# Optimization experiments

Hardware: AMD Instinct MI355X
Metric: run time of the kernel (lower is better)

## Reference

```python
import jax, jax.numpy as jnp
import numpy as np

B, N, F, DM, DMO, OM, L = 32, 64, 64, 128, 64, 128, 4
PRE_H, PRE_O, POST_H = 128, 64, 64
E = N * N
EPS = 1e-5


def swish(x):
    return x * jax.nn.sigmoid(x)


def bn_edges(x, g, b):
    # BatchNorm1d(num_features=E) applied to [B, E, D]: per-edge-channel stats over (batch, D)
    m = x.mean(axis=(0, 2), keepdims=True)
    v = x.var(axis=(0, 2), keepdims=True)
    return (x - m) / jnp.sqrt(v + EPS) * g[None, :, None] + b[None, :, None]


def setup_inputs():
    key = jax.random.key(0)
    ks = iter(jax.random.split(key, 64))

    def rn(shape, s=0.05):
        return jax.random.normal(next(ks), shape, dtype=jnp.float32) * s

    # fully-connected graph incl. self-loops (required by BatchNorm1d(n_nodes^2))
    src, dst = np.meshgrid(np.arange(N), np.arange(N), indexing='ij')
    edge_index = jnp.asarray(np.stack([src.reshape(-1), dst.reshape(-1)]), dtype=jnp.int32)
    return {
        'node_feature': rn((B, N, F), 1.0),
        'vectors': rn((B, N, OM), 1.0),
        'edge_index': edge_index,
        'msg_W1': rn((L, 2 * F, DM)), 'msg_b1': rn((L, DM)),
        'bn1_g': jnp.ones((L, E), jnp.float32), 'bn1_b': jnp.zeros((L, E), jnp.float32),
        'msg_W2': rn((L, DM, DM)), 'msg_b2': rn((L, DM)),
        'bn2_g': jnp.ones((L, E), jnp.float32), 'bn2_b': jnp.zeros((L, E), jnp.float32),
        'msg_W3': rn((L, DM, DM)), 'msg_b3': rn((L, DM)),
        'bn3_g': jnp.ones((L, E), jnp.float32), 'bn3_b': jnp.zeros((L, E), jnp.float32),
        'msg_W4': rn((L, DM, DMO)), 'msg_b4': rn((L, DMO)),
        'upd_W1': rn((L, OM + F + DMO, DM)), 'upd_b1': rn((L, DM)),
        'upd_W2': rn((L, DM, DM)), 'upd_b2': rn((L, DM)),
        'upd_W3': rn((L, DM, DM)), 'upd_b3': rn((L, DM)),
        'upd_W4': rn((L, DM, F)), 'upd_b4': rn((L, F)),
        'pre_W1': rn((F, PRE_H)), 'pre_b1': rn((PRE_H,)),
        'pre_W2': rn((PRE_H, PRE_H)), 'pre_b2': rn((PRE_H,)),
        'pre_W3': rn((PRE_H, PRE_H)), 'pre_b3': rn((PRE_H,)),
        'pre_W4': rn((PRE_H, PRE_O)), 'pre_b4': rn((PRE_O,)),
        'post_W1': rn((PRE_O, POST_H)), 'post_b1': rn((POST_H,)),
        'post_W2': rn((POST_H, 1)), 'post_b2': rn((1,)),
    }


def reference(node_feature, vectors, edge_index,
              msg_W1, msg_b1, bn1_g, bn1_b, msg_W2, msg_b2, bn2_g, bn2_b,
              msg_W3, msg_b3, bn3_g, bn3_b, msg_W4, msg_b4,
              upd_W1, upd_b1, upd_W2, upd_b2, upd_W3, upd_b3, upd_W4, upd_b4,
              pre_W1, pre_b1, pre_W2, pre_b2, pre_W3, pre_b3, pre_W4, pre_b4,
              post_W1, post_b1, post_W2, post_b2):
    src, dst = edge_index[0], edge_index[1]
    x = node_feature  # [B, N, F]
    v = vectors       # [B, N, OM]
    cnt = jax.ops.segment_sum(jnp.ones((E,), jnp.float32), dst, num_segments=N)
    inv_cnt = 1.0 / jnp.maximum(cnt, 1.0)
    for l in range(L):
        x_i = x[:, dst]  # [B, E, F] gather targets
        x_j = x[:, src]  # [B, E, F] gather sources
        h = swish(jnp.concatenate([x_i, x_j], -1) @ msg_W1[l] + msg_b1[l])
        h = bn_edges(h, bn1_g[l], bn1_b[l])
        h = bn_edges(swish(h @ msg_W2[l] + msg_b2[l]), bn2_g[l], bn2_b[l])
        h = bn_edges(swish(h @ msg_W3[l] + msg_b3[l]), bn3_g[l], bn3_b[l])
        m = swish(h @ msg_W4[l] + msg_b4[l])  # [B, E, DMO]
        agg = jax.ops.segment_sum(jnp.transpose(m, (1, 0, 2)), dst, num_segments=N)
        agg = jnp.transpose(agg, (1, 0, 2)) * inv_cnt[None, :, None]  # mean aggr, [B, N, DMO]
        u = jnp.concatenate([v, x, agg], -1)  # [B, N, OM+F+DMO]
        h = swish(u @ upd_W1[l] + upd_b1[l])
        h = swish(h @ upd_W2[l] + upd_b2[l])
        h = swish(h @ upd_W3[l] + upd_b3[l])
        x = x + swish(h @ upd_W4[l] + upd_b4[l])  # residual update
    h = swish(x @ pre_W1 + pre_b1)
    h = swish(h @ pre_W2 + pre_b2)
    h = swish(h @ pre_W3 + pre_b3)
    h = h @ pre_W4 + pre_b4
    c = swish(h @ post_W1 + post_b1) @ post_W2 + post_b2  # [B, N, 1]
    x3 = jnp.einsum('bnd,bn->bd', v, c[..., 0])           # coefficient-weighted vector sum
    return x3, v, c
```

## Files before the change

kernel.cpp:

```cpp
#include <hip/hip_runtime.h>
#include <hip/hip_bf16.h>

typedef unsigned short u16t;
typedef __attribute__((ext_vector_type(8))) short bf16x8;
typedef __attribute__((ext_vector_type(4))) float f32x4;

#define Bn 32
#define Nn 64
#define Fd 64
#define DMd 128
#define DMOd 64
#define OMd 128
#define En 4096

#define NTEN 36
#define TOTALC 1073217
#define HP 136
#define UP 264
#define XP 72
#define WSEG 131072

__device__ const int kOffs[NTEN + 1] = {
    0,        131072,   393216,   458752,   459264,   475648,   492032,   557568,
    558080,   574464,   590848,   656384,   656896,   673280,   689664,   722432,
    722688,   853760,   854272,   919808,   920320,   985856,   986368,   1019136,
    1019392,  1027584,  1027712,  1044096,  1044224,  1060608,  1060736,  1068928,
    1068992,  1073088,  1073152,  1073216,  1073217
};

#define C_NF    0
#define C_VEC   131072
#define C_MW1   393216
#define C_MB1   458752
#define C_G1    459264
#define C_BB1   475648
#define C_MW2   492032
#define C_MB2   557568
#define C_G2    558080
#define C_BB2   574464
#define C_MW3   590848
#define C_MB3   656384
#define C_G3    656896
#define C_BB3   673280
#define C_MW4   689664
#define C_MB4   722432
#define C_UW1   722688
#define C_UB1   853760
#define C_UW2   854272
#define C_UB2   919808
#define C_UW3   920320
#define C_UB3   985856
#define C_UW4   986368
#define C_UB4   1019136
#define C_PW1   1019392
#define C_PB1   1027584
#define C_PW2   1027712
#define C_PB2   1044096
#define C_PW3   1044224
#define C_PB3   1060608
#define C_PW4   1060736
#define C_PB4   1068928
#define C_QW1   1068992
#define C_QB1   1073088
#define C_QW2   1073152
#define C_QB2   1073216

#define S_W2T 0
#define S_W3T 16384
#define S_W4T 32768
#define S_U1T 40960
#define S_U2T 73728
#define S_U3T 90112
#define S_U4T 106496
#define S_W1T 114688

struct Ptrs { const void* p[NTEN]; };

__device__ __forceinline__ float us2f(u16t u) {
    return __uint_as_float(((unsigned int)u) << 16);
}
__device__ __forceinline__ u16t f2us(float f) {
    __hip_bfloat16 h = __float2bfloat16(f);
    return *reinterpret_cast<u16t*>(&h);
}
__device__ __forceinline__ u16t f2us_fast(float f) {
    return (u16t)((__float_as_uint(f) + 0x8000u) >> 16);
}
__device__ __forceinline__ unsigned pack2(float f0, float f1) {
    return __builtin_amdgcn_perm(__float_as_uint(f1) + 0x8000u,
                                 __float_as_uint(f0) + 0x8000u, 0x07060302u);
}
__device__ __forceinline__ float swishf(float x) {
    return x * __builtin_amdgcn_rcpf(1.0f + __expf(-x));
}

__global__ void k_flag(const u16t* __restrict__ g1raw, int* __restrict__ flag) {
    if (threadIdx.x == 0) *flag = (g1raw[0] == 0x3F80u) ? 1 : 0;
}

__global__ __launch_bounds__(256) void k_convert(Ptrs t, float* __restrict__ C,
                                                 float* __restrict__ x,
                                                 const int* __restrict__ flagp) {
    int i = blockIdx.x * 256 + threadIdx.x;
    if (i >= TOTALC) return;
    const int flag = *flagp;
    int lo = 0, hi = NTEN;
    while (hi - lo > 1) { int m = (lo + hi) >> 1; if (i >= kOffs[m]) lo = m; else hi = m; }
    const int local = i - kOffs[lo];
    float v;
    if (flag) v = us2f(((const u16t*)t.p[lo])[local]);
    else      v = ((const float*)t.p[lo])[local];
    C[i] = v;
    if (i < Bn * Nn * Fd) x[i] = v;
}

__global__ __launch_bounds__(256) void k_prepw(const float* __restrict__ C,
                                               u16t* __restrict__ W) {
    int i = blockIdx.x * 256 + threadIdx.x;
    if (i >= 4 * WSEG) return;
    const int l = i / WSEG;
    int r = i - l * WSEG;
    int src;
    if (r < S_W3T)      { int q = r;          int n = q >> 7, k = q & 127; src = C_MW2 + l*16384 + k*128 + n; }
    else if (r < S_W4T) { int q = r - S_W3T;  int n = q >> 7, k = q & 127; src = C_MW3 + l*16384 + k*128 + n; }
    else if (r < S_U1T) { int q = r - S_W4T;  int n = q >> 7, k = q & 127; src = C_MW4 + l*8192  + k*64  + n; }
    else if (r < S_U2T) { int q = r - S_U1T;  int n = q >> 8, k = q & 255; src = C_UW1 + l*32768 + k*128 + n; }
    else if (r < S_U3T) { int q = r - S_U2T;  int n = q >> 7, k = q & 127; src = C_UW2 + l*16384 + k*128 + n; }
    else if (r < S_U4T) { int q = r - S_U3T;  int n = q >> 7, k = q & 127; src = C_UW3 + l*16384 + k*128 + n; }
    else if (r < S_W1T) { int q = r - S_U4T;  int n = q >> 7, k = q & 127; src = C_UW4 + l*8192  + k*64  + n; }
    else                { int q = r - S_W1T;  int n = q >> 7, k = q & 127; src = C_MW1 + l*16384 + k*128 + n; }
    W[i] = f2us(C[src]);
}

__global__ __launch_bounds__(128) void k_pq0(const float* __restrict__ x,
                                             const float* __restrict__ W1,
                                             float* __restrict__ P, float* __restrict__ Q,
                                             float* __restrict__ agg) {
    const int gid = blockIdx.x * 128 + threadIdx.x;
    if (gid < Bn * Nn * DMOd) agg[gid] = 0.f;
    __shared__ float xr[Fd];
    const int bn = blockIdx.x;
    const int tid = threadIdx.x;
    if (tid < Fd) xr[tid] = x[bn * Fd + tid];
    __syncthreads();
    float accP = 0.f, accQ = 0.f;
    #pragma unroll
    for (int k = 0; k < Fd; k++) {
        float xv = xr[k];
        accP += xv * W1[k * DMd + tid];
        accQ += xv * W1[(Fd + k) * DMd + tid];
    }
    P[bn * DMd + tid] = accP;
    Q[bn * DMd + tid] = accQ;
}

__device__ __forceinline__ void red8(float* s, float (*red)[8], float (*stats)[2],
                                     int wv, int lane, int tid) {
    #pragma unroll
    for (int off = 32; off > 0; off >>= 1)
        #pragma unroll
        for (int k = 0; k < 8; k++) s[k] += __shfl_down(s[k], off);
    if (lane == 0) {
        #pragma unroll
        for (int k = 0; k < 8; k++) red[wv][k] = s[k];
    }
    __syncthreads();
    if (tid < 4) {
        float S  = red[0][2*tid]   + red[1][2*tid]   + red[2][2*tid]   + red[3][2*tid];
        float S2 = red[0][2*tid+1] + red[1][2*tid+1] + red[2][2*tid+1] + red[3][2*tid+1];
        float mean = S * (1.0f / 4096.0f);
        float var  = S2 * (1.0f / 4096.0f) - mean * mean;
        stats[tid][0] = mean;
        stats[tid][1] = rsqrtf(var + 1e-5f);
    }
    __syncthreads();
}

__global__ __launch_bounds__(256, 4) void k_edge(
    const float* __restrict__ P, const float* __restrict__ Q,
    const float* __restrict__ b1v,
    const float* __restrict__ g1, const float* __restrict__ bb1,
    const u16t* __restrict__ W2t, const float* __restrict__ b2v,
    const float* __restrict__ g2, const float* __restrict__ bb2,
    const u16t* __restrict__ W3t, const float* __restrict__ b3v,
    const float* __restrict__ g3, const float* __restrict__ bb3,
    const u16t* __restrict__ W4t, const float* __restrict__ b4v,
    float* __restrict__ agg) {
    __shared__ u16t hE[4][Bn * HP];
    __shared__ float red[4][8];
    __shared__ float stats[4][2];

    const int dst = blockIdx.x & 63, src0 = (blockIdx.x >> 6) * 4;
    const int tid = threadIdx.x;
    const int wv = tid >> 6, lane = tid & 63, quad = lane >> 4, l15 = lane & 15;
    const int mw = wv & 1, nb2 = wv >> 1;
    const int mrow = mw * 16 + l15;
    const int nBase = nb2 * 64;

    {
        const int b = tid >> 3, d0 = (tid & 7) * 16;
        float4 pv[4], bv[4];
        {
            const float4* pp = (const float4*)&P[(b * Nn + dst) * DMd + d0];
            const float4* bp = (const float4*)&b1v[d0];
            #pragma unroll
            for (int j = 0; j < 4; j++) { pv[j] = pp[j]; bv[j] = bp[j]; }
        }
        float h[4][16];
        #pragma unroll
        for (int e = 0; e < 4; e++) {
            const float4* qq = (const float4*)&Q[(b * Nn + src0 + e) * DMd + d0];
            #pragma unroll
            for (int j = 0; j < 4; j++) {
                float4 qv = qq[j];
                h[e][j*4+0] = swishf(pv[j].x + qv.x + bv[j].x);
                h[e][j*4+1] = swishf(pv[j].y + qv.y + bv[j].y);
                h[e][j*4+2] = swishf(pv[j].z + qv.z + bv[j].z);
                h[e][j*4+3] = swishf(pv[j].w + qv.w + bv[j].w);
            }
        }
        float s[8];
        #pragma unroll
        for (int e = 0; e < 4; e++) {
            float se = 0.f, s2e = 0.f;
            #pragma unroll
            for (int i = 0; i < 16; i++) { se += h[e][i]; s2e += h[e][i] * h[e][i]; }
            s[2*e] = se; s[2*e+1] = s2e;
        }
        red8(s, red, stats, wv, lane, tid);
        #pragma unroll
        for (int e = 0; e < 4; e++) {
            float a  = stats[e][1] * g1[(src0 + e) * Nn + dst];
            float cc = bb1[(src0 + e) * Nn + dst] - stats[e][0] * a;
            uint4 w0, w1;
            w0.x = pack2(h[e][0]  * a + cc, h[e][1]  * a + cc);
            w0.y = pack2(h[e][2]  * a + cc, h[e][3]  * a + cc);
            w0.z = pack2(h[e][4]  * a + cc, h[e][5]  * a + cc);
            w0.w = pack2(h[e][6]  * a + cc, h[e][7]  * a + cc);
            w1.x = pack2(h[e][8]  * a + cc, h[e][9]  * a + cc);
            w1.y = pack2(h[e][10] * a + cc, h[e][11] * a + cc);
            w1.z = pack2(h[e][12] * a + cc, h[e][13] * a + cc);
            w1.w = pack2(h[e][14] * a + cc, h[e][15] * a + cc);
            *(uint4*)&hE[e][b * HP + d0]     = w0;
            *(uint4*)&hE[e][b * HP + d0 + 8] = w1;
        }
    }
    __syncthreads();

    #pragma unroll 1
    for (int st = 0; st < 2; st++) {
        const u16t*  Wt = st ? W3t : W2t;
        const float* bv = st ? b3v : b2v;
        const float* gv = st ? g3  : g2;
        const float* bb = st ? bb3 : bb2;
        f32x4 acc[4][4];
        #pragma unroll
        for (int t = 0; t < 4; t++) {
            float b0 = bv[nBase + t * 16 + l15];
            #pragma unroll
            for (int e = 0; e < 4; e++) acc[e][t] = (f32x4){b0, b0, b0, b0};
        }
        #pragma unroll
        for (int ks = 0; ks < 4; ks++) {
            bf16x8 wb[4];
            #pragma unroll
            for (int t = 0; t < 4; t++)
                wb[t] = *(const bf16x8*)&Wt[(nBase + t * 16 + l15) * 128 + ks * 32 + quad * 8];
            #pragma unroll
            for (int e = 0; e < 4; e++) {
                bf16x8 a8 = *(const bf16x8*)&hE[e][mrow * HP + ks * 32 + quad * 8];
                #pragma unroll
                for (int t = 0; t < 4; t++)
                    acc[e][t] = __builtin_amdgcn_mfma_f32_16x16x32_bf16(a8, wb[t], acc[e][t], 0, 0, 0);
            }
        }
        float s[8];
        #pragma unroll
        for (int e = 0; e < 4; e++) {
            float se = 0.f, s2e = 0.f;
            #pragma unroll
            for (int t = 0; t < 4; t++)
                #pragma unroll
                for (int r = 0; r < 4; r++) {
                    float v = swishf(acc[e][t][r]);
                    acc[e][t][r] = v;
                    se += v; s2e += v * v;
                }
            s[2*e] = se; s[2*e+1] = s2e;
        }
        red8(s, red, stats, wv, lane, tid);
        #pragma unroll
        for (int e = 0; e < 4; e++) {
            float a  = stats[e][1] * gv[(src0 + e) * Nn + dst];
            float cc = bb[(src0 + e) * Nn + dst] - stats[e][0] * a;
            #pragma unroll
            for (int t = 0; t < 4; t++)
                #pragma unroll
                for (int r = 0; r < 4; r++)
                    hE[e][(mw * 16 + quad * 4 + r) * HP + nBase + t * 16 + l15] =
                        f2us_fast(acc[e][t][r] * a + cc);
        }
        __syncthreads();
    }

    {
        const int n40 = nb2 * 32;
        f32x4 a4[4][2];
        #pragma unroll
        for (int t = 0; t < 2; t++) {
            float b0 = b4v[n40 + t * 16 + l15];
            #pragma unroll
            for (int e = 0; e < 4; e++) a4[e][t] = (f32x4){b0, b0, b0, b0};
        }
        #pragma unroll
        for (int ks = 0; ks < 4; ks++) {
            bf16x8 wb[2];
            #pragma unroll
            for (int t = 0; t < 2; t++)
                wb[t] = *(const bf16x8*)&W4t[(n40 + t * 16 + l15) * 128 + ks * 32 + quad * 8];
            #pragma unroll
            for (int e = 0; e < 4; e++) {
                bf16x8 a8 = *(const bf16x8*)&hE[e][mrow * HP + ks * 32 + quad * 8];
                #pragma unroll
                for (int t = 0; t < 2; t++)
                    a4[e][t] = __builtin_amdgcn_mfma_f32_16x16x32_bf16(a8, wb[t], a4[e][t], 0, 0, 0);
            }
        }
        #pragma unroll
        for (int t = 0; t < 2; t++)
            #pragma unroll
            for (int r = 0; r < 4; r++) {
                float m = swishf(a4[0][t][r]) + swishf(a4[1][t][r])
                        + swishf(a4[2][t][r]) + swishf(a4[3][t][r]);
                int b = mw * 16 + quad * 4 + r;
                atomicAdd(&agg[(b * Nn + dst) * DMOd + n40 + t * 16 + l15], m);
            }
    }
}

__global__ __launch_bounds__(256, 4) void k_updq(
    const float* __restrict__ vC, float* __restrict__ x, float* __restrict__ agg,
    const u16t* __restrict__ U1t, const float* __restrict__ b1,
    const u16t* __restrict__ U2t, const float* __restrict__ b2,
    const u16t* __restrict__ U3t, const float* __restrict__ b3,
    const u16t* __restrict__ U4t, const float* __restrict__ b4,
    const u16t* __restrict__ W1Tn, float* __restrict__ Pn, float* __restrict__ Qn,
    int doPQ) {
    __shared__ u16t uL[16 * UP];
    __shared__ u16t hL[16 * HP];
    __shared__ u16t xL[16 * XP];
    const int g0 = blockIdx.x * 16;
    const int tid = threadIdx.x;
    const int wv = tid >> 6, lane = tid & 63, quad = lane >> 4, l15 = lane & 15;
    const int nBase = wv * 32;

    {
        const int i = tid >> 4, c0 = (tid & 15) * 16;
        const int g = g0 + i;
        const float* srcp; float scl = 1.f;
        if (c0 < 128)       srcp = &vC[g * OMd + c0];
        else if (c0 < 192)  srcp = &x[g * Fd + (c0 - 128)];
        else              { srcp = &agg[g * DMOd + (c0 - 192)]; scl = 1.0f / 64.0f; }
        uint4 s0, s1;
        s0.x = pack2(srcp[0]  * scl, srcp[1]  * scl);
        s0.y = pack2(srcp[2]  * scl, srcp[3]  * scl);
        s0.z = pack2(srcp[4]  * scl, srcp[5]  * scl);
        s0.w = pack2(srcp[6]  * scl, srcp[7]  * scl);
        s1.x = pack2(srcp[8]  * scl, srcp[9]  * scl);
        s1.y = pack2(srcp[10] * scl, srcp[11] * scl);
        s1.z = pack2(srcp[12] * scl, srcp[13] * scl);
        s1.w = pack2(srcp[14] * scl, srcp[15] * scl);
        *(uint4*)&uL[i * UP + c0]     = s0;
        *(uint4*)&uL[i * UP + c0 + 8] = s1;
    }
    __syncthreads();

    {
        f32x4 acc[2];
        #pragma unroll
        for (int t = 0; t < 2; t++) {
            float b0 = b1[nBase + t * 16 + l15];
            acc[t] = (f32x4){b0, b0, b0, b0};
        }
        #pragma unroll
        for (int ks = 0; ks < 8; ks++) {
            bf16x8 a8 = *(const bf16x8*)&uL[l15 * UP + ks * 32 + quad * 8];
            #pragma unroll
            for (int t = 0; t < 2; t++) {
                bf16x8 b8 = *(const bf16x8*)&U1t[(nBase + t * 16 + l15) * 256 + ks * 32 + quad * 8];
                acc[t] = __builtin_amdgcn_mfma_f32_16x16x32_bf16(a8, b8, acc[t], 0, 0, 0);
            }
        }
        #pragma unroll
        for (int t = 0; t < 2; t++)
            #pragma unroll
            for (int r = 0; r < 4; r++)
                hL[(quad * 4 + r) * HP + nBase + t * 16 + l15] = f2us_fast(swishf(acc[t][r]));
    }
    __syncthreads();

    #pragma unroll 1
    for (int st = 0; st < 2; st++) {
        const u16t*  Ut = st ? U3t : U2t;
        const float* bb = st ? b3  : b2;
        f32x4 acc[2];
        #pragma unroll
        for (int t = 0; t < 2; t++) {
            float b0 = bb[nBase + t * 16 + l15];
            acc[t] = (f32x4){b0, b0, b0, b0};
        }
        #pragma unroll
        for (int ks = 0; ks < 4; ks++) {
            bf16x8 a8 = *(const bf16x8*)&hL[l15 * HP + ks * 32 + quad * 8];
            #pragma unroll
            for (int t = 0; t < 2; t++) {
                bf16x8 b8 = *(const bf16x8*)&Ut[(nBase + t * 16 + l15) * 128 + ks * 32 + quad * 8];
                acc[t] = __builtin_amdgcn_mfma_f32_16x16x32_bf16(a8, b8, acc[t], 0, 0, 0);
            }
        }
        __syncthreads();
        #pragma unroll
        for (int t = 0; t < 2; t++)
            #pragma unroll
            for (int r = 0; r < 4; r++)
                hL[(quad * 4 + r) * HP + nBase + t * 16 + l15] = f2us_fast(swishf(acc[t][r]));
        __syncthreads();
    }

    {
        const int n4 = wv * 16;
        f32x4 acc;
        {
            float b0 = b4[n4 + l15];
            acc = (f32x4){b0, b0, b0, b0};
        }
        #pragma unroll
        for (int ks = 0; ks < 4; ks++) {
            bf16x8 a8 = *(const bf16x8*)&hL[l15 * HP + ks * 32 + quad * 8];
            bf16x8 b8 = *(const bf16x8*)&U4t[(n4 + l15) * 128 + ks * 32 + quad * 8];
            acc = __builtin_amdgcn_mfma_f32_16x16x32_bf16(a8, b8, acc, 0, 0, 0);
        }
        #pragma unroll
        for (int r = 0; r < 4; r++) {
            int row = quad * 4 + r, col = n4 + l15;
            float xn = x[(g0 + row) * Fd + col] + swishf(acc[r]);
            x[(g0 + row) * Fd + col] = xn;
            xL[row * XP + col] = f2us_fast(xn);
        }
    }

    {
        int idx = tid;
        #pragma unroll
        for (int k = 0; k < 4; k++, idx += 256) agg[g0 * DMOd + idx] = 0.f;
    }
    __syncthreads();

    if (doPQ) {
        f32x4 ap[2], aq[2];
        #pragma unroll
        for (int j = 0; j < 2; j++) { ap[j] = (f32x4){0,0,0,0}; aq[j] = (f32x4){0,0,0,0}; }
        #pragma unroll
        for (int ks = 0; ks < 2; ks++) {
            bf16x8 a8 = *(const bf16x8*)&xL[l15 * XP + ks * 32 + quad * 8];
            #pragma unroll
            for (int j = 0; j < 2; j++) {
                const int n0 = (wv * 2 + j) * 16 + l15;
                bf16x8 bp = *(const bf16x8*)&W1Tn[n0 * 128 + ks * 32 + quad * 8];
                bf16x8 bq = *(const bf16x8*)&W1Tn[n0 * 128 + 64 + ks * 32 + quad * 8];
                ap[j] = __builtin_amdgcn_mfma_f32_16x16x32_bf16(a8, bp, ap[j], 0, 0, 0);
                aq[j] = __builtin_amdgcn_mfma_f32_16x16x32_bf16(a8, bq, aq[j], 0, 0, 0);
            }
        }
        #pragma unroll
        for (int j = 0; j < 2; j++)
            #pragma unroll
            for (int r = 0; r < 4; r++) {
                int g = g0 + quad * 4 + r, col = (wv * 2 + j) * 16 + l15;
                Pn[g * DMd + col] = ap[j][r];
                Qn[g * DMd + col] = aq[j][r];
            }
    }
}

__global__ __launch_bounds__(128) void k_final(
    const float* __restrict__ x, const void* __restrict__ vraw,
    const float* __restrict__ pW1, const float* __restrict__ pb1,
    const float* __restrict__ pW2, const float* __restrict__ pb2,
    const float* __restrict__ pW3, const float* __restrict__ pb3,
    const float* __restrict__ pW4, const float* __restrict__ pb4,
    const float* __restrict__ qW1, const float* __restrict__ qb1,
    const float* __restrict__ qW2, const float* __restrict__ qb2,
    float* __restrict__ c_buf, void* __restrict__ out, const int* __restrict__ flagp) {
    __shared__ float xr[64];
    __shared__ float ha[128];
    __shared__ float hb[128];
    __shared__ float hc[64];
    __shared__ float tt[64];
    const int bn = blockIdx.x;
    const int tid = threadIdx.x;
    const int flag = *flagp;
    if (tid < 64) xr[tid] = x[bn * Fd + tid];
    __syncthreads();
    float acc = pb1[tid];
    #pragma unroll 8
    for (int k = 0; k < 64; k++) acc += xr[k] * pW1[k * 128 + tid];
    ha[tid] = swishf(acc);
    __syncthreads();
    acc = pb2[tid];
    #pragma unroll 8
    for (int k = 0; k < 128; k++) acc += ha[k] * pW2[k * 128 + tid];
    hb[tid] = swishf(acc);
    __syncthreads();
    acc = pb3[tid];
    #pragma unroll 8
    for (int k = 0; k < 128; k++) acc += hb[k] * pW3[k * 128 + tid];
    ha[tid] = swishf(acc);
    __syncthreads();
    if (tid < 64) {
        acc = pb4[tid];
        #pragma unroll 8
        for (int k = 0; k < 128; k++) acc += ha[k] * pW4[k * 64 + tid];
        hc[tid] = acc;
    }
    __syncthreads();
    if (tid < 64) {
        acc = qb1[tid];
        #pragma unroll 8
        for (int k = 0; k < 64; k++) acc += hc[k] * qW1[k * 64 + tid];
        tt[tid] = swishf(acc);
    }
    __syncthreads();
    if (tid < 64) {
        float p = tt[tid] * qW2[tid];
        #pragma unroll
        for (int off = 32; off > 0; off >>= 1) p += __shfl_down(p, off);
        if (tid == 0) {
            float cv = p + qb2[0];
            c_buf[bn] = cv;
            const int ci = 4096 + Bn * Nn * OMd + bn;
            if (flag) ((u16t*)out)[ci] = f2us(cv);
            else      ((float*)out)[ci] = cv;
        }
    }
    const int vi = bn * OMd + tid;
    if (flag) ((u16t*)out)[4096 + vi] = ((const u16t*)vraw)[vi];
    else      ((float*)out)[4096 + vi] = ((const float*)vraw)[vi];
}

__global__ __launch_bounds__(128) void k_x3(const float* __restrict__ vC,
                                            const float* __restrict__ c_buf,
                                            void* __restrict__ out,
                                            const int* __restrict__ flagp) {
    const int b = blockIdx.x, d = threadIdx.x;
    const int flag = *flagp;
    float acc = 0.f;
    #pragma unroll 4
    for (int n = 0; n < Nn; n++)
        acc += vC[(b * Nn + n) * OMd + d] * c_buf[b * Nn + n];
    if (flag) ((u16t*)out)[b * OMd + d] = f2us(acc);
    else      ((float*)out)[b * OMd + d] = acc;
}

extern "C" void kernel_launch(void* const* d_in, const int* in_sizes, int n_in,
                              void* d_out, int out_size, void* d_ws, size_t ws_size,
                              hipStream_t stream) {
    float* ws = (float*)d_ws;
    int*   flag  = (int*)d_ws;
    float* C     = ws + 16;
    float* x     = C + 1073664;
    float* P     = x + 131072;
    float* Q     = P + 262144;
    float* agg   = Q + 262144;
    float* c_buf = agg + 131072;
    u16t*  Wt    = (u16t*)(c_buf + 2048);

    Ptrs t;
    for (int i = 0, j = 0; i < 37; i++) {
        if (i == 2) continue;
        t.p[j++] = d_in[i];
    }

    k_flag<<<1, 64, 0, stream>>>((const u16t*)d_in[5], flag);
    k_convert<<<(TOTALC + 255) / 256, 256, 0, stream>>>(t, C, x, flag);
    k_prepw<<<(4 * WSEG + 255) / 256, 256, 0, stream>>>(C, Wt);
    k_pq0<<<Bn * Nn, 128, 0, stream>>>(x, C + C_MW1, P, Q, agg);

    for (int l = 0; l < 4; l++) {
        u16t* Wl = Wt + l * WSEG;
        k_edge<<<64 * 16, 256, 0, stream>>>(
            P, Q,
            C + C_MB1 + l * DMd, C + C_G1 + l * En, C + C_BB1 + l * En,
            Wl + S_W2T, C + C_MB2 + l * DMd, C + C_G2 + l * En, C + C_BB2 + l * En,
            Wl + S_W3T, C + C_MB3 + l * DMd, C + C_G3 + l * En, C + C_BB3 + l * En,
            Wl + S_W4T, C + C_MB4 + l * DMOd,
            agg);
        const int doPQ = (l < 3) ? 1 : 0;
        const u16t* W1Tn = Wt + (doPQ ? (l + 1) : 0) * WSEG + S_W1T;
        k_updq<<<Bn * Nn / 16, 256, 0, stream>>>(
            C + C_VEC, x, agg,
            Wl + S_U1T, C + C_UB1 + l * DMd,
            Wl + S_U2T, C + C_UB2 + l * DMd,
            Wl + S_U3T, C + C_UB3 + l * DMd,
            Wl + S_U4T, C + C_UB4 + l * DMOd,
            W1Tn, P, Q, doPQ);
    }

    k_final<<<Bn * Nn, 128, 0, stream>>>(x, d_in[1],
        C + C_PW1, C + C_PB1, C + C_PW2, C + C_PB2,
        C + C_PW3, C + C_PB3, C + C_PW4, C + C_PB4,
        C + C_QW1, C + C_QB1, C + C_QW2, C + C_QB2,
        c_buf, d_out, flag);
    k_x3<<<Bn, 128, 0, stream>>>(C + C_VEC, c_buf, d_out, flag);
}
```

Measured before the change: 451.1 us.

## Replace atomic aggregation with per-source-group partial buffers reduced in update kernel

The edge kernel now writes each source-group's message sum to its own slice of a partial buffer instead of doing atomicAdd into a shared aggregation array. The update kernel sums the 16 partial slices into shared memory before building its input, so the separate zeroing of agg is no longer needed. This removes atomic contention and the zeroing passes. In exchange it adds a 16x larger scratch buffer (8 MB) and extra global reads in the update kernel.

Result: slower. 467.0 us (+3.5%).

```diff
diff --git a/kernel.cpp b/kernel.cpp
--- a/kernel.cpp
+++ b/kernel.cpp
@@ -134,10 +134,7 @@
 
 __global__ __launch_bounds__(128) void k_pq0(const float* __restrict__ x,
                                              const float* __restrict__ W1,
-                                             float* __restrict__ P, float* __restrict__ Q,
-                                             float* __restrict__ agg) {
-    const int gid = blockIdx.x * 128 + threadIdx.x;
-    if (gid < Bn * Nn * DMOd) agg[gid] = 0.f;
+                                             float* __restrict__ P, float* __restrict__ Q) {
     __shared__ float xr[Fd];
     const int bn = blockIdx.x;
     const int tid = threadIdx.x;
@@ -185,12 +182,12 @@
     const u16t* __restrict__ W3t, const float* __restrict__ b3v,
     const float* __restrict__ g3, const float* __restrict__ bb3,
     const u16t* __restrict__ W4t, const float* __restrict__ b4v,
-    float* __restrict__ agg) {
+    float* __restrict__ m_part) {
     __shared__ u16t hE[4][Bn * HP];
     __shared__ float red[4][8];
     __shared__ float stats[4][2];
 
-    const int dst = blockIdx.x & 63, src0 = (blockIdx.x >> 6) * 4;
+    const int dst = blockIdx.x & 63, sg = blockIdx.x >> 6, src0 = sg * 4;
     const int tid = threadIdx.x;
     const int wv = tid >> 6, lane = tid & 63, quad = lane >> 4, l15 = lane & 15;
     const int mw = wv & 1, nb2 = wv >> 1;
@@ -333,13 +330,14 @@
                 float m = swishf(a4[0][t][r]) + swishf(a4[1][t][r])
                         + swishf(a4[2][t][r]) + swishf(a4[3][t][r]);
                 int b = mw * 16 + quad * 4 + r;
-                atomicAdd(&agg[(b * Nn + dst) * DMOd + n40 + t * 16 + l15], m);
+                m_part[(size_t)sg * (Bn * Nn * DMOd) + b * (Nn * DMOd) + dst * DMOd
+                       + n40 + t * 16 + l15] = m;
             }
     }
 }
 
 __global__ __launch_bounds__(256, 4) void k_updq(
-    const float* __restrict__ vC, float* __restrict__ x, float* __restrict__ agg,
+    const float* __restrict__ vC, float* __restrict__ x, const float* __restrict__ m_part,
     const u16t* __restrict__ U1t, const float* __restrict__ b1,
     const u16t* __restrict__ U2t, const float* __restrict__ b2,
     const u16t* __restrict__ U3t, const float* __restrict__ b3,
@@ -349,10 +347,26 @@
     __shared__ u16t uL[16 * UP];
     __shared__ u16t hL[16 * HP];
     __shared__ u16t xL[16 * XP];
-    const int g0 = blockIdx.x * 16;
+    __shared__ float aggL[16 * 64];
+    const int bl = blockIdx.x;
+    const int g0 = bl * 16;
     const int tid = threadIdx.x;
     const int wv = tid >> 6, lane = tid & 63, quad = lane >> 4, l15 = lane & 15;
     const int nBase = wv * 32;
+
+    {
+        const int bb = bl >> 2, j0 = (bl & 3) * 16;
+        const int o = tid * 4;
+        const float* base = m_part + (size_t)bb * (Nn * DMOd) + (j0 + (o >> 6)) * DMOd + (o & 63);
+        float4 s = *(const float4*)base;
+        #pragma unroll
+        for (int sgi = 1; sgi < 16; sgi++) {
+            float4 v = *(const float4*)(base + (size_t)sgi * (Bn * Nn * DMOd));
+            s.x += v.x; s.y += v.y; s.z += v.z; s.w += v.w;
+        }
+        *(float4*)&aggL[o] = s;
+    }
+    __syncthreads();
 
     {
         const int i = tid >> 4, c0 = (tid & 15) * 16;
@@ -360,7 +374,7 @@
         const float* srcp; float scl = 1.f;
         if (c0 < 128)       srcp = &vC[g * OMd + c0];
         else if (c0 < 192)  srcp = &x[g * Fd + (c0 - 128)];
-        else              { srcp = &agg[g * DMOd + (c0 - 192)]; scl = 1.0f / 64.0f; }
+        else              { srcp = &aggL[i * 64 + (c0 - 192)]; scl = 1.0f / 64.0f; }
         uint4 s0, s1;
         s0.x = pack2(srcp[0]  * scl, srcp[1]  * scl);
         s0.y = pack2(srcp[2]  * scl, srcp[3]  * scl);
@@ -447,12 +461,6 @@
             x[(g0 + row) * Fd + col] = xn;
             xL[row * XP + col] = f2us_fast(xn);
         }
-    }
-
-    {
-        int idx = tid;
-        #pragma unroll
-        for (int k = 0; k < 4; k++, idx += 256) agg[g0 * DMOd + idx] = 0.f;
     }
     __syncthreads();
 
@@ -566,14 +574,14 @@
                               void* d_out, int out_size, void* d_ws, size_t ws_size,
                               hipStream_t stream) {
     float* ws = (float*)d_ws;
-    int*   flag  = (int*)d_ws;
-    float* C     = ws + 16;
-    float* x     = C + 1073664;
-    float* P     = x + 131072;
-    float* Q     = P + 262144;
-    float* agg   = Q + 262144;
-    float* c_buf = agg + 131072;
-    u16t*  Wt    = (u16t*)(c_buf + 2048);
+    int*   flag   = (int*)d_ws;
+    float* C      = ws + 16;
+    float* x      = C + 1073664;
+    float* P      = x + 131072;
+    float* Q      = P + 262144;
+    float* m_part = Q + 262144;
+    float* c_buf  = m_part + 2097152;
+    u16t*  Wt     = (u16t*)(c_buf + 2048);
 
     Ptrs t;
     for (int i = 0, j = 0; i < 37; i++) {
@@ -584,7 +592,7 @@
     k_flag<<<1, 64, 0, stream>>>((const u16t*)d_in[5], flag);
     k_convert<<<(TOTALC + 255) / 256, 256, 0, stream>>>(t, C, x, flag);
     k_prepw<<<(4 * WSEG + 255) / 256, 256, 0, stream>>>(C, Wt);
-    k_pq0<<<Bn * Nn, 128, 0, stream>>>(x, C + C_MW1, P, Q, agg);
+    k_pq0<<<Bn * Nn, 128, 0, stream>>>(x, C + C_MW1, P, Q);
 
     for (int l = 0; l < 4; l++) {
         u16t* Wl = Wt + l * WSEG;
@@ -594,11 +602,11 @@
             Wl + S_W2T, C + C_MB2 + l * DMd, C + C_G2 + l * En, C + C_BB2 + l * En,
             Wl + S_W3T, C + C_MB3 + l * DMd, C + C_G3 + l * En, C + C_BB3 + l * En,
             Wl + S_W4T, C + C_MB4 + l * DMOd,
-            agg);
+            m_part);
         const int doPQ = (l < 3) ? 1 : 0;
         const u16t* W1Tn = Wt + (doPQ ? (l + 1) : 0) * WSEG + S_W1T;
         k_updq<<<Bn * Nn / 16, 256, 0, stream>>>(
-            C + C_VEC, x, agg,
+            C + C_VEC, x, m_part,
             Wl + S_U1T, C + C_UB1 + l * DMd,
             Wl + S_U2T, C + C_UB2 + l * DMd,
             Wl + S_U3T, C + C_UB3 + l * DMd,
```
